# Performance work log

Hardware: AMD Instinct MI355X
Metric: run time of the kernel (lower is better)

Reference implementation:

```python
import jax, jax.numpy as jnp
import numpy as np

N, IN_DIM, OUT_DIM, HEADS = 8192, 256, 64, 2

def setup_inputs() -> dict:
    key = jax.random.key(0)
    k1, k2, k3, k4, k5 = jax.random.split(key, 5)
    x = jax.random.normal(k1, (N, IN_DIM), dtype=jnp.float32)
    adj = jax.random.randint(k2, (N, N), 0, 2, dtype=jnp.int32)
    # nn.Linear(in_dim, out_dim*heads, bias=False): weight [out_dim*heads, in_dim]
    W = jax.random.normal(k3, (OUT_DIM * HEADS, IN_DIM), dtype=jnp.float32) / np.sqrt(IN_DIM)
    attn_l = jax.random.normal(k4, (HEADS, OUT_DIM), dtype=jnp.float32)
    attn_r = jax.random.normal(k5, (HEADS, OUT_DIM), dtype=jnp.float32)
    return {"x": x, "adj": adj, "W": W, "attn_l": attn_l, "attn_r": attn_r}

def reference(x, adj, W, attn_l, attn_r):
    n = x.shape[0]
    h = (x @ W.T).reshape(n, HEADS, OUT_DIM)          # [N, H, D]
    el = jnp.einsum('nhd,hd->nh', h, attn_l)           # [N, H]
    er = jnp.einsum('nhd,hd->nh', h, attn_r)           # [N, H]
    e = el[:, None, :] + er[None, :, :]                # [N, N, H]
    e = jnp.where(adj[:, :, None] == 0, -jnp.inf, e)
    a = jax.nn.softmax(e, axis=1)                      # softmax over source nodes j
    out = jnp.einsum('ijh,jhd->ihd', a, h)             # [N, H, D]
    return out.reshape(n, HEADS * OUT_DIM)
```

## Files before the change

### kernel.cpp

```cpp
#include <hip/hip_runtime.h>
#include <cstdint>
#include <cstddef>

#define N_NODES 8192
#define IN_DIM  256
#define OUT_DIM 64
#define HEADS   2
#define FEAT    128
#define NTILES  9
#define ACC_STRIDE 132
#define KSPLIT  8

typedef __bf16 bf16x8 __attribute__((ext_vector_type(8)));
typedef float  f32x4  __attribute__((ext_vector_type(4)));
typedef int    i32x4  __attribute__((ext_vector_type(4)));
typedef unsigned uu32x4 __attribute__((ext_vector_type(4)));

static __device__ __forceinline__ unsigned short f2bf(float f) {
  unsigned u = __float_as_uint(f);
  u += 0x7FFFu + ((u >> 16) & 1u);
  return (unsigned short)(u >> 16);
}

__global__ __launch_bounds__(256) void k_prep(const float* __restrict__ x,
                                              const float* __restrict__ W,
                                              const float* __restrict__ attn_r,
                                              uint4* __restrict__ frag) {
  const int kb = blockIdx.x;
  const int tid = threadIdx.x;
  const int tx = tid & 15, ty = tid >> 4;
  const int j0 = kb * 32;

  __shared__ float xs[32][68];
  __shared__ float wl[128][68];
  __shared__ unsigned short pk[32][146];

  float acc[2][8] = {};

  for (int kc = 0; kc < IN_DIM; kc += 64) {
    __syncthreads();
#pragma unroll
    for (int p = 0; p < 2; p++) {
      const int slot = p*256 + tid;
      const int r = slot >> 4, k4 = slot & 15;
      *(float4*)&xs[r][k4*4] = *(const float4*)(x + (size_t)(j0 + r)*IN_DIM + kc + k4*4);
    }
#pragma unroll
    for (int p = 0; p < 8; p++) {
      const int slot = p*256 + tid;
      const int r = slot >> 4, k4 = slot & 15;
      *(float4*)&wl[r][k4*4] = *(const float4*)(W + (size_t)r*IN_DIM + kc + k4*4);
    }
    __syncthreads();
#pragma unroll
    for (int k4 = 0; k4 < 16; k4++) {
      float4 xr[2], wr[8];
#pragma unroll
      for (int i = 0; i < 2; i++) xr[i] = *(const float4*)&xs[ty + i*16][k4*4];
#pragma unroll
      for (int jj = 0; jj < 8; jj++) wr[jj] = *(const float4*)&wl[tx + jj*16][k4*4];
#pragma unroll
      for (int i = 0; i < 2; i++)
#pragma unroll
        for (int jj = 0; jj < 8; jj++)
          acc[i][jj] += xr[i].x*wr[jj].x + xr[i].y*wr[jj].y +
                        xr[i].z*wr[jj].z + xr[i].w*wr[jj].w;
    }
  }

  float ar[8];
#pragma unroll
  for (int jj = 0; jj < 8; jj++)
    ar[jj] = attn_r[((jj >> 2)) * OUT_DIM + ((tx + jj*16) & 63)];
  float e0[2] = {}, e1[2] = {};
#pragma unroll
  for (int i = 0; i < 2; i++) {
#pragma unroll
    for (int jj = 0; jj < 4; jj++) e0[i] += acc[i][jj] * ar[jj];
#pragma unroll
    for (int jj = 4; jj < 8; jj++) e1[i] += acc[i][jj] * ar[jj];
  }
#pragma unroll
  for (int m = 1; m <= 8; m <<= 1) {
#pragma unroll
    for (int i = 0; i < 2; i++) {
      e0[i] += __shfl_xor(e0[i], m);
      e1[i] += __shfl_xor(e1[i], m);
    }
  }
  float w0[2], w1[2];
#pragma unroll
  for (int i = 0; i < 2; i++) { w0[i] = __expf(e0[i]); w1[i] = __expf(e1[i]); }

#pragma unroll
  for (int i = 0; i < 2; i++) {
    const int row = ty + i*16;
#pragma unroll
    for (int jj = 0; jj < 8; jj++)
      pk[row][tx + jj*16] = f2bf((jj < 4 ? w0[i] : w1[i]) * acc[i][jj]);
    pk[row][128 + tx] = (tx == 0) ? f2bf(w0[i]) : (tx == 1) ? f2bf(w1[i]) : 0;
  }
  __syncthreads();

#pragma unroll
  for (int t = 0; t < 3; t++) {
    const int wid = t*256 + tid;
    if (wid < 576) {
      const int l = wid & 63, n = wid >> 6;
      const int col = n*16 + (l & 15), jb = (l >> 4) * 8;
      uint4 o;
      o.x = (unsigned)pk[jb+0][col] | ((unsigned)pk[jb+1][col] << 16);
      o.y = (unsigned)pk[jb+2][col] | ((unsigned)pk[jb+3][col] << 16);
      o.z = (unsigned)pk[jb+4][col] | ((unsigned)pk[jb+5][col] << 16);
      o.w = (unsigned)pk[jb+6][col] | ((unsigned)pk[jb+7][col] << 16);
      frag[((size_t)kb*NTILES + n)*64 + l] = o;
    }
  }
}

__global__ __launch_bounds__(256, 2) void k_main(const int* __restrict__ adj,
                                                 const uint4* __restrict__ fragB,
                                                 float* __restrict__ accum) {
  const int mb = blockIdx.x >> 3;
  const int ks = blockIdx.x & 7;
  const int tid = threadIdx.x;
  const int wave = tid >> 6, lane = tid & 63;
  const int m16 = lane & 15, quad = lane >> 4;

  __shared__ int tile[4][4096];

  const int lr = lane >> 3;
  const int lc = ((lane & 7) ^ lr) << 2;
  const int* gbase = adj + (size_t)(mb*128)*N_NODES + ks*1024 + (size_t)lr*N_NODES + lc;

  auto stage = [&](int buf, int kk) {
#pragma unroll
    for (int i = 0; i < 4; ++i) {
      const int c = wave*4 + i;
      const int* g = gbase + (size_t)(c*8)*N_NODES + kk*32;
      __builtin_amdgcn_global_load_lds(
        (const __attribute__((address_space(1))) void*)g,
        (__attribute__((address_space(3))) void*)&tile[buf][c*256],
        16, 0, 0);
    }
  };

  const int r0 = wave*32 + m16;
  const int swz = (r0 & 7) << 4;
  const int a0off = r0*128 + ((quad*32) ^ swz);
  const uu32x4* bb = (const uu32x4*)fragB + (size_t)(ks*32)*NTILES*64 + lane;

  f32x4 acc0[NTILES], acc1[NTILES];
#pragma unroll
  for (int n = 0; n < NTILES; n++) {
    acc0[n] = (f32x4){0.f, 0.f, 0.f, 0.f};
    acc1[n] = (f32x4){0.f, 0.f, 0.f, 0.f};
  }

  uu32x4 bvA[NTILES], bvB[NTILES];

  auto loadB = [&](int kk, uu32x4* bv) {
#pragma unroll
    for (int t = 0; t < NTILES; t++)
      bv[t] = bb[(size_t)kk*NTILES*64 + (size_t)t*64];
  };
  auto conv8 = [&](i32x4 lo, i32x4 hi) -> bf16x8 {
    unsigned u0 = (lo[0] ? 0x3F80u : 0u) | (lo[1] ? 0x3F800000u : 0u);
    unsigned u1 = (lo[2] ? 0x3F80u : 0u) | (lo[3] ? 0x3F800000u : 0u);
    unsigned u2 = (hi[0] ? 0x3F80u : 0u) | (hi[1] ? 0x3F800000u : 0u);
    unsigned u3 = (hi[2] ? 0x3F80u : 0u) | (hi[3] ? 0x3F800000u : 0u);
    uu32x4 u = {u0, u1, u2, u3};
    return __builtin_bit_cast(bf16x8, u);
  };
  auto substep = [&](int buf, const uu32x4* bv) {
    const char* tb = (const char*)&tile[0][0] + buf*16384;
    i32x4 x00 = *(const i32x4*)(tb + a0off);
    i32x4 x01 = *(const i32x4*)(tb + (a0off ^ 16));
    i32x4 x10 = *(const i32x4*)(tb + a0off + 2048);
    i32x4 x11 = *(const i32x4*)(tb + (a0off ^ 16) + 2048);
    bf16x8 af0 = conv8(x00, x01);
    bf16x8 af1 = conv8(x10, x11);
#pragma unroll
    for (int n = 0; n < NTILES; n++) {
      bf16x8 bfr = __builtin_bit_cast(bf16x8, bv[n]);
      acc0[n] = __builtin_amdgcn_mfma_f32_16x16x32_bf16(af0, bfr, acc0[n], 0, 0, 0);
    }
#pragma unroll
    for (int n = 0; n < NTILES; n++) {
      bf16x8 bfr = __builtin_bit_cast(bf16x8, bv[n]);
      acc1[n] = __builtin_amdgcn_mfma_f32_16x16x32_bf16(af1, bfr, acc1[n], 0, 0, 0);
    }
  };

  stage(0, 0);
  stage(1, 1);
  loadB(0, bvA);
  asm volatile("s_waitcnt vmcnt(13)" ::: "memory");
  __builtin_amdgcn_s_barrier();

  for (int k = 0; k < 32; k += 4) {
#pragma unroll
    for (int j = 0; j < 4; ++j) {
      const int kk = k + j;
      if (kk + 2 < 32) stage((kk + 2) & 3, kk + 2);
      if (kk + 1 < 32) loadB(kk + 1, (j & 1) ? bvA : bvB);
      substep(kk & 3, (j & 1) ? bvB : bvA);
      asm volatile("s_waitcnt vmcnt(13)" ::: "memory");
      __builtin_amdgcn_s_barrier();
    }
  }

  const int rb0 = mb*128 + wave*32 + quad*4;
  float* op = accum + (size_t)ks*N_NODES*ACC_STRIDE;
#pragma unroll
  for (int n = 0; n < NTILES; n++) {
    if (n == 8 && m16 >= HEADS) continue;
#pragma unroll
    for (int r = 0; r < 4; r++) {
      op[(size_t)(rb0 + r)*ACC_STRIDE + n*16 + m16]      = acc0[n][r];
      op[(size_t)(rb0 + 16 + r)*ACC_STRIDE + n*16 + m16] = acc1[n][r];
    }
  }
}

__global__ void k_div(const float* __restrict__ acc, float* __restrict__ out) {
  const int tid = threadIdx.x;
  const int r = tid >> 5, c4 = (tid & 31) << 2;
  const int i = blockIdx.x * 8 + r;
  const int h = c4 >> 6;
  f32x4 num = (f32x4){0.f, 0.f, 0.f, 0.f};
  float den = 0.f;
#pragma unroll
  for (int s = 0; s < KSPLIT; s++) {
    const float* p = acc + ((size_t)s*N_NODES + i)*ACC_STRIDE;
    num += *(const f32x4*)(p + c4);
    den += p[FEAT + h];
  }
  f32x4 o = num / (f32x4){den, den, den, den};
  *(f32x4*)(out + (size_t)i*FEAT + c4) = o;
}

extern "C" void kernel_launch(void* const* d_in, const int* in_sizes, int n_in,
                              void* d_out, int out_size, void* d_ws, size_t ws_size,
                              hipStream_t stream) {
  const float* x      = (const float*)d_in[0];
  const int*   adj    = (const int*)  d_in[1];
  const float* W      = (const float*)d_in[2];
  const float* attn_r = (const float*)d_in[4];

  char* ws = (char*)d_ws;
  uint4* frag = (uint4*)(ws + 0);
  float* acc  = (float*)(ws + 4194304);
  float* out  = (float*)d_out;

  hipLaunchKernelGGL(k_prep, dim3(256),  dim3(256), 0, stream, x, W, attn_r, frag);
  hipLaunchKernelGGL(k_main, dim3(512),  dim3(256), 0, stream, adj, frag, acc);
  hipLaunchKernelGGL(k_div,  dim3(1024), dim3(256), 0, stream, acc, out);
}
```

Baseline: 429.1 us.

## Stage B fragments through LDS and double waves per block in main kernel

The main kernel now runs 8 waves per block, each owning 16 rows instead of 32. The shared B fragments are brought into LDS with async global_load_lds alongside the adjacency tiles, replacing per-wave register double-buffering from global memory. The adj loads also get a cache-policy bit. This cuts redundant B global traffic and register pressure to raise occupancy, at the cost of extra LDS reads per MFMA and more waves hitting barriers.

```diff
diff --git a/kernel.cpp b/kernel.cpp
--- a/kernel.cpp
+++ b/kernel.cpp
@@ -118,7 +118,7 @@
   }
 }
 
-__global__ __launch_bounds__(256, 2) void k_main(const int* __restrict__ adj,
+__global__ __launch_bounds__(512, 2) void k_main(const int* __restrict__ adj,
                                                  const uint4* __restrict__ fragB,
                                                  float* __restrict__ accum) {
   const int mb = blockIdx.x >> 3;
@@ -127,43 +127,44 @@
   const int wave = tid >> 6, lane = tid & 63;
   const int m16 = lane & 15, quad = lane >> 4;
 
-  __shared__ int tile[4][4096];
+  __shared__ int   tA[4][4096];
+  __shared__ uint4 tB[4][576];
 
   const int lr = lane >> 3;
   const int lc = ((lane & 7) ^ lr) << 2;
-  const int* gbase = adj + (size_t)(mb*128)*N_NODES + ks*1024 + (size_t)lr*N_NODES + lc;
-
-  auto stage = [&](int buf, int kk) {
-#pragma unroll
-    for (int i = 0; i < 4; ++i) {
-      const int c = wave*4 + i;
-      const int* g = gbase + (size_t)(c*8)*N_NODES + kk*32;
+  const int* gA = adj + (size_t)(mb*128)*N_NODES + ks*1024 + (size_t)lr*N_NODES + lc;
+
+  const uint4* gB = fragB + (size_t)(ks*32)*576 + lane;
+
+  auto stageA = [&](int slot, int kk) {
+#pragma unroll
+    for (int i = 0; i < 2; ++i) {
+      const int c = wave*2 + i;
+      const int* g = gA + (size_t)(c*8)*N_NODES + kk*32;
       __builtin_amdgcn_global_load_lds(
         (const __attribute__((address_space(1))) void*)g,
-        (__attribute__((address_space(3))) void*)&tile[buf][c*256],
-        16, 0, 0);
-    }
-  };
-
-  const int r0 = wave*32 + m16;
+        (__attribute__((address_space(3))) void*)&tA[slot][c*256], 16, 0, 2 );
+    }
+  };
+  auto stageB = [&](int slot, int kk) {
+    const uint4* g = gB + (size_t)kk*576;
+    __builtin_amdgcn_global_load_lds(
+      (const __attribute__((address_space(1))) void*)(g + wave*64),
+      (__attribute__((address_space(3))) void*)&tB[slot][wave*64], 16, 0, 0);
+    if (wave == 0)
+      __builtin_amdgcn_global_load_lds(
+        (const __attribute__((address_space(1))) void*)(g + 8*64),
+        (__attribute__((address_space(3))) void*)&tB[slot][8*64], 16, 0, 0);
+  };
+
+  const int r0 = wave*16 + m16;
   const int swz = (r0 & 7) << 4;
   const int a0off = r0*128 + ((quad*32) ^ swz);
-  const uu32x4* bb = (const uu32x4*)fragB + (size_t)(ks*32)*NTILES*64 + lane;
-
-  f32x4 acc0[NTILES], acc1[NTILES];
-#pragma unroll
-  for (int n = 0; n < NTILES; n++) {
-    acc0[n] = (f32x4){0.f, 0.f, 0.f, 0.f};
-    acc1[n] = (f32x4){0.f, 0.f, 0.f, 0.f};
-  }
-
-  uu32x4 bvA[NTILES], bvB[NTILES];
-
-  auto loadB = [&](int kk, uu32x4* bv) {
-#pragma unroll
-    for (int t = 0; t < NTILES; t++)
-      bv[t] = bb[(size_t)kk*NTILES*64 + (size_t)t*64];
-  };
+
+  f32x4 acc[NTILES];
+#pragma unroll
+  for (int n = 0; n < NTILES; n++) acc[n] = (f32x4){0.f, 0.f, 0.f, 0.f};
+
   auto conv8 = [&](i32x4 lo, i32x4 hi) -> bf16x8 {
     unsigned u0 = (lo[0] ? 0x3F80u : 0u) | (lo[1] ? 0x3F800000u : 0u);
     unsigned u1 = (lo[2] ? 0x3F80u : 0u) | (lo[3] ? 0x3F800000u : 0u);
@@ -172,54 +173,47 @@
     uu32x4 u = {u0, u1, u2, u3};
     return __builtin_bit_cast(bf16x8, u);
   };
-  auto substep = [&](int buf, const uu32x4* bv) {
-    const char* tb = (const char*)&tile[0][0] + buf*16384;
-    i32x4 x00 = *(const i32x4*)(tb + a0off);
-    i32x4 x01 = *(const i32x4*)(tb + (a0off ^ 16));
-    i32x4 x10 = *(const i32x4*)(tb + a0off + 2048);
-    i32x4 x11 = *(const i32x4*)(tb + (a0off ^ 16) + 2048);
-    bf16x8 af0 = conv8(x00, x01);
-    bf16x8 af1 = conv8(x10, x11);
+  auto compute = [&](int slot) {
+    const char* ta = (const char*)&tA[slot][0];
+    i32x4 x0 = *(const i32x4*)(ta + a0off);
+    i32x4 x1 = *(const i32x4*)(ta + (a0off ^ 16));
+    bf16x8 af = conv8(x0, x1);
+    const uu32x4* bp = (const uu32x4*)&tB[slot][0] + lane;
 #pragma unroll
     for (int n = 0; n < NTILES; n++) {
-      bf16x8 bfr = __builtin_bit_cast(bf16x8, bv[n]);
-      acc0[n] = __builtin_amdgcn_mfma_f32_16x16x32_bf16(af0, bfr, acc0[n], 0, 0, 0);
-    }
-#pragma unroll
-    for (int n = 0; n < NTILES; n++) {
-      bf16x8 bfr = __builtin_bit_cast(bf16x8, bv[n]);
-      acc1[n] = __builtin_amdgcn_mfma_f32_16x16x32_bf16(af1, bfr, acc1[n], 0, 0, 0);
-    }
-  };
-
-  stage(0, 0);
-  stage(1, 1);
-  loadB(0, bvA);
-  asm volatile("s_waitcnt vmcnt(13)" ::: "memory");
+      bf16x8 bfr = __builtin_bit_cast(bf16x8, bp[n*64]);
+      acc[n] = __builtin_amdgcn_mfma_f32_16x16x32_bf16(af, bfr, acc[n], 0, 0, 0);
+    }
+  };
+
+  stageA(0, 0); stageB(0, 0);
+  stageA(1, 1); stageB(1, 1);
+  if (wave == 0) asm volatile("s_waitcnt vmcnt(4)" ::: "memory");
+  else           asm volatile("s_waitcnt vmcnt(3)" ::: "memory");
   __builtin_amdgcn_s_barrier();
-
-  for (int k = 0; k < 32; k += 4) {
-#pragma unroll
-    for (int j = 0; j < 4; ++j) {
-      const int kk = k + j;
-      if (kk + 2 < 32) stage((kk + 2) & 3, kk + 2);
-      if (kk + 1 < 32) loadB(kk + 1, (j & 1) ? bvA : bvB);
-      substep(kk & 3, (j & 1) ? bvB : bvA);
-      asm volatile("s_waitcnt vmcnt(13)" ::: "memory");
-      __builtin_amdgcn_s_barrier();
-    }
-  }
-
-  const int rb0 = mb*128 + wave*32 + quad*4;
+  __builtin_amdgcn_sched_barrier(0);
+
+  for (int kk = 0; kk < 32; ++kk) {
+    if (kk + 2 < 32) { stageA((kk + 2) & 3, kk + 2); stageB((kk + 2) & 3, kk + 2); }
+    compute(kk & 3);
+    if (kk < 30) {
+      if (wave == 0) asm volatile("s_waitcnt vmcnt(4)" ::: "memory");
+      else           asm volatile("s_waitcnt vmcnt(3)" ::: "memory");
+    } else {
+      asm volatile("s_waitcnt vmcnt(0)" ::: "memory");
+    }
+    __builtin_amdgcn_s_barrier();
+    __builtin_amdgcn_sched_barrier(0);
+  }
+
+  const int rb0 = mb*128 + wave*16 + quad*4;
   float* op = accum + (size_t)ks*N_NODES*ACC_STRIDE;
 #pragma unroll
   for (int n = 0; n < NTILES; n++) {
     if (n == 8 && m16 >= HEADS) continue;
 #pragma unroll
-    for (int r = 0; r < 4; r++) {
-      op[(size_t)(rb0 + r)*ACC_STRIDE + n*16 + m16]      = acc0[n][r];
-      op[(size_t)(rb0 + 16 + r)*ACC_STRIDE + n*16 + m16] = acc1[n][r];
-    }
+    for (int r = 0; r < 4; r++)
+      op[(size_t)(rb0 + r)*ACC_STRIDE + n*16 + m16] = acc[n][r];
   }
 }
 
@@ -254,6 +248,6 @@
   float* out  = (float*)d_out;
 
   hipLaunchKernelGGL(k_prep, dim3(256),  dim3(256), 0, stream, x, W, attn_r, frag);
-  hipLaunchKernelGGL(k_main, dim3(512),  dim3(256), 0, stream, adj, frag, acc);
+  hipLaunchKernelGGL(k_main, dim3(512),  dim3(512), 0, stream, adj, frag, acc);
   hipLaunchKernelGGL(k_div,  dim3(1024), dim3(256), 0, stream, acc, out);
 }
```

Measured after the change: 419.6 us. -2.2%, faster.

## Pre-pack adjacency into bitmask and drop LDS staging in main kernel

Applied to the files above, without the earlier changes.

Adds a streaming pass, fused into the prep kernel's grid, that reads the int32 adjacency matrix once with nontemporal loads and writes a 1-bit-per-entry mask. The main MFMA kernel then reads these compact bit words straight into registers and expands them to bf16 fragments, removing the LDS tiles, async global-to-LDS loads and per-step barriers. This targets the main kernel's latency- and occupancy-bound handling of the 256MB adjacency read. In exchange it adds an extra 8MB write and read of the mask plus a separate pass, and the prefetch runs one group past each split's slice.

```diff
diff --git a/kernel.cpp b/kernel.cpp
--- a/kernel.cpp
+++ b/kernel.cpp
@@ -10,6 +10,7 @@
 #define NTILES  9
 #define ACC_STRIDE 132
 #define KSPLIT  8
+#define PACK_BLOCKS 2048
 
 typedef __bf16 bf16x8 __attribute__((ext_vector_type(8)));
 typedef float  f32x4  __attribute__((ext_vector_type(4)));
@@ -22,18 +23,40 @@
   return (unsigned short)(u >> 16);
 }
 
-__global__ __launch_bounds__(256) void k_prep(const float* __restrict__ x,
-                                              const float* __restrict__ W,
-                                              const float* __restrict__ attn_r,
-                                              uint4* __restrict__ frag) {
-  const int kb = blockIdx.x;
-  const int tid = threadIdx.x;
-  const int tx = tid & 15, ty = tid >> 4;
-  const int j0 = kb * 32;
-
+__global__ __launch_bounds__(256) void k_prep_pack(const float* __restrict__ x,
+                                                   const float* __restrict__ W,
+                                                   const float* __restrict__ attn_r,
+                                                   const int* __restrict__ adj,
+                                                   uint4* __restrict__ frag,
+                                                   unsigned* __restrict__ bm) {
   __shared__ float xs[32][68];
   __shared__ float wl[128][68];
   __shared__ unsigned short pk[32][146];
+
+  const int tid = threadIdx.x;
+
+  if (blockIdx.x < PACK_BLOCKS) {
+#pragma unroll
+    for (int rr = 0; rr < 4; ++rr) {
+      const int row = blockIdx.x * 4 + rr;
+      const i32x4* p = (const i32x4*)(adj + (size_t)row * N_NODES) + tid * 8;
+      unsigned w = 0;
+#pragma unroll
+      for (int i = 0; i < 8; ++i) {
+        i32x4 v = __builtin_nontemporal_load(p + i);
+        w |= (v[0] != 0 ? 1u : 0u) << (i*4 + 0);
+        w |= (v[1] != 0 ? 1u : 0u) << (i*4 + 1);
+        w |= (v[2] != 0 ? 1u : 0u) << (i*4 + 2);
+        w |= (v[3] != 0 ? 1u : 0u) << (i*4 + 3);
+      }
+      bm[(size_t)row * 256 + tid] = w;
+    }
+    return;
+  }
+
+  const int kb = blockIdx.x - PACK_BLOCKS;
+  const int tx = tid & 15, ty = tid >> 4;
+  const int j0 = kb * 32;
 
   float acc[2][8] = {};
 
@@ -118,7 +141,7 @@
   }
 }
 
-__global__ __launch_bounds__(256, 2) void k_main(const int* __restrict__ adj,
+__global__ __launch_bounds__(256, 2) void k_main(const unsigned* __restrict__ bm,
                                                  const uint4* __restrict__ fragB,
                                                  float* __restrict__ accum) {
   const int mb = blockIdx.x >> 3;
@@ -127,27 +150,9 @@
   const int wave = tid >> 6, lane = tid & 63;
   const int m16 = lane & 15, quad = lane >> 4;
 
-  __shared__ int tile[4][4096];
-
-  const int lr = lane >> 3;
-  const int lc = ((lane & 7) ^ lr) << 2;
-  const int* gbase = adj + (size_t)(mb*128)*N_NODES + ks*1024 + (size_t)lr*N_NODES + lc;
-
-  auto stage = [&](int buf, int kk) {
-#pragma unroll
-    for (int i = 0; i < 4; ++i) {
-      const int c = wave*4 + i;
-      const int* g = gbase + (size_t)(c*8)*N_NODES + kk*32;
-      __builtin_amdgcn_global_load_lds(
-        (const __attribute__((address_space(1))) void*)g,
-        (__attribute__((address_space(3))) void*)&tile[buf][c*256],
-        16, 0, 0);
-    }
-  };
-
-  const int r0 = wave*32 + m16;
-  const int swz = (r0 & 7) << 4;
-  const int a0off = r0*128 + ((quad*32) ^ swz);
+  const int row0 = mb*128 + wave*32 + m16;
+  const i32x4* a0p = (const i32x4*)bm + (size_t)row0*64 + ks*8;
+  const i32x4* a1p = a0p + (size_t)16*64;
   const uu32x4* bb = (const uu32x4*)fragB + (size_t)(ks*32)*NTILES*64 + lane;
 
   f32x4 acc0[NTILES], acc1[NTILES];
@@ -159,55 +164,49 @@
 
   uu32x4 bvA[NTILES], bvB[NTILES];
 
-  auto loadB = [&](int kk, uu32x4* bv) {
-#pragma unroll
-    for (int t = 0; t < NTILES; t++)
-      bv[t] = bb[(size_t)kk*NTILES*64 + (size_t)t*64];
-  };
-  auto conv8 = [&](i32x4 lo, i32x4 hi) -> bf16x8 {
-    unsigned u0 = (lo[0] ? 0x3F80u : 0u) | (lo[1] ? 0x3F800000u : 0u);
-    unsigned u1 = (lo[2] ? 0x3F80u : 0u) | (lo[3] ? 0x3F800000u : 0u);
-    unsigned u2 = (hi[0] ? 0x3F80u : 0u) | (hi[1] ? 0x3F800000u : 0u);
-    unsigned u3 = (hi[2] ? 0x3F80u : 0u) | (hi[3] ? 0x3F800000u : 0u);
+  auto unpack = [&](unsigned wbits) -> bf16x8 {
+    const unsigned b = (wbits >> (quad * 8)) & 0xFFu;
+    unsigned u0 = (b & 1u   ? 0x3F80u : 0u) | (b & 2u   ? 0x3F800000u : 0u);
+    unsigned u1 = (b & 4u   ? 0x3F80u : 0u) | (b & 8u   ? 0x3F800000u : 0u);
+    unsigned u2 = (b & 16u  ? 0x3F80u : 0u) | (b & 32u  ? 0x3F800000u : 0u);
+    unsigned u3 = (b & 64u  ? 0x3F80u : 0u) | (b & 128u ? 0x3F800000u : 0u);
     uu32x4 u = {u0, u1, u2, u3};
     return __builtin_bit_cast(bf16x8, u);
   };
-  auto substep = [&](int buf, const uu32x4* bv) {
-    const char* tb = (const char*)&tile[0][0] + buf*16384;
-    i32x4 x00 = *(const i32x4*)(tb + a0off);
-    i32x4 x01 = *(const i32x4*)(tb + (a0off ^ 16));
-    i32x4 x10 = *(const i32x4*)(tb + a0off + 2048);
-    i32x4 x11 = *(const i32x4*)(tb + (a0off ^ 16) + 2048);
-    bf16x8 af0 = conv8(x00, x01);
-    bf16x8 af1 = conv8(x10, x11);
-#pragma unroll
-    for (int n = 0; n < NTILES; n++) {
-      bf16x8 bfr = __builtin_bit_cast(bf16x8, bv[n]);
-      acc0[n] = __builtin_amdgcn_mfma_f32_16x16x32_bf16(af0, bfr, acc0[n], 0, 0, 0);
-    }
-#pragma unroll
-    for (int n = 0; n < NTILES; n++) {
-      bf16x8 bfr = __builtin_bit_cast(bf16x8, bv[n]);
-      acc1[n] = __builtin_amdgcn_mfma_f32_16x16x32_bf16(af1, bfr, acc1[n], 0, 0, 0);
-    }
-  };
-
-  stage(0, 0);
-  stage(1, 1);
-  loadB(0, bvA);
-  asm volatile("s_waitcnt vmcnt(13)" ::: "memory");
-  __builtin_amdgcn_s_barrier();
-
-  for (int k = 0; k < 32; k += 4) {
+
+  i32x4 aC0 = a0p[0], aC1 = a1p[0];
+#pragma unroll
+  for (int t = 0; t < NTILES; t++) bvA[t] = bb[(size_t)t*64];
+
+  for (int g = 0; g < 8; ++g) {
+    i32x4 aN0 = a0p[g + 1];
+    i32x4 aN1 = a1p[g + 1];
 #pragma unroll
     for (int j = 0; j < 4; ++j) {
-      const int kk = k + j;
-      if (kk + 2 < 32) stage((kk + 2) & 3, kk + 2);
-      if (kk + 1 < 32) loadB(kk + 1, (j & 1) ? bvA : bvB);
-      substep(kk & 3, (j & 1) ? bvB : bvA);
-      asm volatile("s_waitcnt vmcnt(13)" ::: "memory");
-      __builtin_amdgcn_s_barrier();
-    }
+      const int kk = g*4 + j;
+      const uu32x4* bp = bb + (size_t)(kk + 1)*NTILES*64;
+      if ((j & 1) == 0) {
+#pragma unroll
+        for (int t = 0; t < NTILES; t++) bvB[t] = bp[(size_t)t*64];
+      } else {
+#pragma unroll
+        for (int t = 0; t < NTILES; t++) bvA[t] = bp[(size_t)t*64];
+      }
+      bf16x8 af0 = unpack((unsigned)aC0[j]);
+      bf16x8 af1 = unpack((unsigned)aC1[j]);
+      const uu32x4* bv = ((j & 1) == 0) ? bvA : bvB;
+#pragma unroll
+      for (int n = 0; n < NTILES; n++) {
+        bf16x8 bfr = __builtin_bit_cast(bf16x8, bv[n]);
+        acc0[n] = __builtin_amdgcn_mfma_f32_16x16x32_bf16(af0, bfr, acc0[n], 0, 0, 0);
+      }
+#pragma unroll
+      for (int n = 0; n < NTILES; n++) {
+        bf16x8 bfr = __builtin_bit_cast(bf16x8, bv[n]);
+        acc1[n] = __builtin_amdgcn_mfma_f32_16x16x32_bf16(af1, bfr, acc1[n], 0, 0, 0);
+      }
+    }
+    aC0 = aN0; aC1 = aN1;
   }
 
   const int rb0 = mb*128 + wave*32 + quad*4;
@@ -249,11 +248,13 @@
   const float* attn_r = (const float*)d_in[4];
 
   char* ws = (char*)d_ws;
-  uint4* frag = (uint4*)(ws + 0);
-  float* acc  = (float*)(ws + 4194304);
-  float* out  = (float*)d_out;
-
-  hipLaunchKernelGGL(k_prep, dim3(256),  dim3(256), 0, stream, x, W, attn_r, frag);
-  hipLaunchKernelGGL(k_main, dim3(512),  dim3(256), 0, stream, adj, frag, acc);
+  uint4*    frag = (uint4*)(ws + 0);
+  unsigned* bm   = (unsigned*)(ws + (4u << 20));
+  float*    acc  = (float*)(ws + (16u << 20));
+  float*    out  = (float*)d_out;
+
+  hipLaunchKernelGGL(k_prep_pack, dim3(PACK_BLOCKS + 256), dim3(256), 0, stream,
+                     x, W, attn_r, adj, frag, bm);
+  hipLaunchKernelGGL(k_main, dim3(512),  dim3(256), 0, stream, bm, frag, acc);
   hipLaunchKernelGGL(k_div,  dim3(1024), dim3(256), 0, stream, acc, out);
 }
```

Measured after the change: 488.5 us. 1.14x slower.
